# Optimization experiments

Measured on AMD Instinct MI355X. Metric: run time of the kernel, lower is better.

Reference implementation:

```python
import jax, jax.numpy as jnp
import numpy as np

R = 12          # resolution (H = W = G); L = R**3 = 1728
HEADS = 12


def setup_inputs() -> dict:
    key = jax.random.key(0)
    k1, k2, k3 = jax.random.split(key, 3)
    B, L, C = 4, R ** 3, 768
    qkv = jax.random.normal(k1, (3, B, L, C), dtype=jnp.float32)
    lepe_w = jax.random.normal(k2, (C, 1, 3, 3, 3), dtype=jnp.float32) * 0.05
    lepe_b = jax.random.normal(k3, (C,), dtype=jnp.float32) * 0.01
    return {"qkv": qkv, "lepe_w": lepe_w, "lepe_b": lepe_b}


def reference(qkv, lepe_w, lepe_b):
    # qkv: [3, B, L, C]; idx=0 => window == full volume, so attention is dense over L.
    q, k, v = qkv[0], qkv[1], qkv[2]
    B, L, C = q.shape
    hd = C // HEADS
    scale = hd ** -0.5

    # im2cswin with full-volume window preserves token order: [B, L, C] -> [B, H, L, d]
    qh = q.reshape(B, L, HEADS, hd).transpose(0, 2, 1, 3)
    kh = k.reshape(B, L, HEADS, hd).transpose(0, 2, 1, 3)

    # get_lepe: v -> [B, C, R, R, R], depthwise 3x3x3 conv (groups=C)
    v_img = v.transpose(0, 2, 1).reshape(B, C, R, R, R)
    lepe = jax.lax.conv_general_dilated(
        v_img, lepe_w, window_strides=(1, 1, 1), padding="SAME",
        dimension_numbers=("NCDHW", "OIDHW", "NCDHW"), feature_group_count=C,
    ) + lepe_b[None, :, None, None, None]
    lepe = lepe.reshape(B, HEADS, hd, L).transpose(0, 1, 3, 2)   # [B, H, L, d]
    vh = v_img.reshape(B, HEADS, hd, L).transpose(0, 1, 3, 2)    # [B, H, L, d]

    attn = jax.nn.softmax(jnp.einsum("bhqd,bhkd->bhqk", qh * scale, kh), axis=-1)
    out = jnp.einsum("bhqk,bhkd->bhqd", attn, vh) + lepe          # [B, H, L, d]

    # windows2img with full window is an inverse reshape back to [B, L, C]
    return out.transpose(0, 2, 1, 3).reshape(B, L, C)
```

## Files before the change

### kernel.cpp

```cpp
#include <hip/hip_runtime.h>

#define RR 12
#define LL 1728
#define CC 768
#define HEADS 12
#define HD 64
#define BATCH 4

typedef __attribute__((ext_vector_type(8))) short bf8;
typedef __attribute__((ext_vector_type(4))) float f4;

__device__ inline unsigned short f2bf(float x) {
  unsigned int u = __float_as_uint(x);
  return (unsigned short)((u + 0x7FFFu + ((u >> 16) & 1u)) >> 16);
}
__device__ inline unsigned short f2bfr(float x) {
  return (unsigned short)((__float_as_uint(x) + 0x8000u) >> 16);
}

__device__ inline float fast_exp2(float x) {
#if __has_builtin(__builtin_amdgcn_exp2f)
  return __builtin_amdgcn_exp2f(x);
#else
  return exp2f(x);
#endif
}

__device__ inline void gld16(const unsigned short* g, unsigned short* l) {
  __builtin_amdgcn_global_load_lds((const __attribute__((address_space(1))) unsigned int*)g,
                                   (__attribute__((address_space(3))) unsigned int*)l, 16, 0, 0);
}

#define QSCALE 0.1803368801111244f

#define NLEPE 5184
#define NPREP 1296

__global__ __launch_bounds__(256) void combined_kernel(const float* __restrict__ qkv,
                                                       const float* __restrict__ w,
                                                       const float* __restrict__ bias,
                                                       unsigned short* __restrict__ qb,
                                                       unsigned short* __restrict__ kb,
                                                       unsigned short* __restrict__ vT,
                                                       float* __restrict__ out) {
  __shared__ __align__(16) unsigned char smem[27648];
  const int bid = blockIdx.x;
  const int t = threadIdx.x;

  if (bid < NLEPE) {
    const int xg = (bid % 3) * 4;
    const int line = (bid / 3) % 144;
    const int ct = (bid / 432) % 3;
    const int b = bid / 1296;
    const int z = line / RR;
    const int y = line % RR;
    const int c0 = ct * 256;
    const int c = c0 + t;
    float* w_lds = (float*)smem;

    {
      const float* wsrc = w + (size_t)c0 * 27;
#pragma unroll
      for (int i = 0; i < 7; ++i) {
        const int idx = i * 256 + t;
        if (idx < 1728) *(float4*)&w_lds[idx * 4] = *(const float4*)&wsrc[idx * 4];
      }
    }
    __syncthreads();
    float wreg[27];
#pragma unroll
    for (int j = 0; j < 27; ++j) wreg[j] = w_lds[t * 27 + j];

    const float* vb = qkv + ((size_t)(2 * BATCH + b)) * LL * CC + c;
    const float bv = bias[c];
    float acc[4] = {bv, bv, bv, bv};

#pragma unroll
    for (int dz = -1; dz <= 1; ++dz) {
#pragma unroll
      for (int dy = -1; dy <= 1; ++dy) {
        const int zz = z + dz, yy = y + dy;
        const bool lineok = ((unsigned)zz < RR) & ((unsigned)yy < RR);
        const int base = (zz * RR + yy) * RR;
        float v6[6];
#pragma unroll
        for (int p = 0; p < 6; ++p) {
          const int xx = xg - 1 + p;
          const bool ok = lineok & ((unsigned)xx < RR);
          const int lp = ok ? base + xx : 0;
          const float vv = vb[(size_t)lp * CC];
          v6[p] = ok ? vv : 0.f;
        }
        const int jb = ((dz + 1) * 3 + (dy + 1)) * 3;
        const float wL = wreg[jb], wC = wreg[jb + 1], wR = wreg[jb + 2];
#pragma unroll
        for (int i = 0; i < 4; ++i)
          acc[i] += wL * v6[i] + wC * v6[i + 1] + wR * v6[i + 2];
      }
    }
    const size_t obase = ((size_t)b * LL + line * RR + xg) * CC + c;
#pragma unroll
    for (int i = 0; i < 4; ++i) out[obase + (size_t)i * CC] = acc[i];

  } else {
    const int p = bid - NLEPE;
    const int lt = p % 27;
    const int h = (p / 27) % HEADS;
    const int b = p / (27 * HEADS);
    unsigned short* tl = (unsigned short*)smem;

    {
      const int r0 = t >> 4;
      const int c4 = (t & 15) * 4;
#pragma unroll
      for (int pi = 0; pi < 4; ++pi) {
        const int row = lt * 64 + pi * 16 + r0;
        const size_t off = ((size_t)b * LL + row) * CC + h * HD + c4;
        const float4 qv = *(const float4*)(qkv + off);
        ushort4 oq;
        oq.x = f2bf(qv.x * QSCALE); oq.y = f2bf(qv.y * QSCALE);
        oq.z = f2bf(qv.z * QSCALE); oq.w = f2bf(qv.w * QSCALE);
        *(ushort4*)(qb + off) = oq;
        const float4 kv = *(const float4*)(qkv + (size_t)BATCH * LL * CC + off);
        ushort4 ok;
        ok.x = f2bf(kv.x); ok.y = f2bf(kv.y); ok.z = f2bf(kv.z); ok.w = f2bf(kv.w);
        *(ushort4*)(kb + off) = ok;
      }
    }

    const float* vsrc = qkv + ((size_t)(2 * BATCH + b)) * LL * CC;
#pragma unroll
    for (int it = 0; it < 4; ++it) {
      const int idx = it * 256 + t;
      const int lrow = idx >> 4;
      const int c4 = (idx & 15) * 4;
      const float4 vv = *(const float4*)(vsrc + (size_t)(lt * 64 + lrow) * CC + h * HD + c4);
      tl[(c4 + 0) * 65 + lrow] = f2bf(vv.x);
      tl[(c4 + 1) * 65 + lrow] = f2bf(vv.y);
      tl[(c4 + 2) * 65 + lrow] = f2bf(vv.z);
      tl[(c4 + 3) * 65 + lrow] = f2bf(vv.w);
    }
    __syncthreads();
#pragma unroll
    for (int it = 0; it < 4; ++it) {
      const int idx = it * 256 + t;
      const int drow = idx >> 4;
      const int u = idx & 15;
      const int s4 = u * 4;
      const int kbase = (((u >> 3) * 2 + (u & 1)) << 4) + (((u >> 1) & 3) << 2);
      ushort4 o;
      o.x = tl[drow * 65 + kbase + 0];
      o.y = tl[drow * 65 + kbase + 1];
      o.z = tl[drow * 65 + kbase + 2];
      o.w = tl[drow * 65 + kbase + 3];
      *(ushort4*)(vT + (((size_t)(b * HEADS + h) * HD + drow) * LL) + lt * 64 + s4) = o;
    }
  }
}

__global__ __launch_bounds__(256) void attn_kernel(const unsigned short* __restrict__ qb,
                                                   const unsigned short* __restrict__ kb,
                                                   const unsigned short* __restrict__ vT,
                                                   float* __restrict__ out) {
  __shared__ unsigned short k_lds[2][64 * 64];
  __shared__ unsigned short v_lds[2][64 * 64];

  const int qt = blockIdx.x;
  const int h = blockIdx.y;
  const int b = blockIdx.z;
  const int t = threadIdx.x;
  const int lane = t & 63;
  const int wave = t >> 6;
  const int m = lane & 15;
  const int quad = lane >> 4;

  bf8 qf[2];
  {
    const size_t qbase = ((size_t)(b * LL + qt * 64 + wave * 16 + m)) * CC + h * HD;
    qf[0] = *(const bf8*)(qb + qbase + quad * 8);
    qf[1] = *(const bf8*)(qb + qbase + 32 + quad * 8);
  }

  int koff[2], voff[2], ldsb[2];
#pragma unroll
  for (int j = 0; j < 2; ++j) {
    const int cidx = (j * 4 + wave) * 64 + lane;
    const int row = cidx >> 3;
    const int sc = (cidx & 7) ^ (row & 7);
    koff[j] = row * CC + sc * 8;
    voff[j] = row * LL + sc * 8;
    ldsb[j] = (j * 4 + wave) * 512;
  }

  const unsigned short* kgb = kb + (size_t)b * LL * CC + h * HD;
  const unsigned short* vgb = vT + ((size_t)(b * HEADS + h) * HD) * LL;

  gld16(kgb + koff[0], &k_lds[0][ldsb[0]]);
  gld16(kgb + koff[1], &k_lds[0][ldsb[1]]);
  gld16(vgb + voff[0], &v_lds[0][ldsb[0]]);
  gld16(vgb + voff[1], &v_lds[0][ldsb[1]]);

  f4 o_acc[4] = {};
  float psum = 0.f;

#define ATTN_BODY(KT, CUR)                                                              \
  {                                                                                     \
    __syncthreads();            \
    if ((KT) < 26) {                                                                    \
      const size_t ko = (size_t)((KT) + 1) * 64 * CC;                                   \
      const int vo = ((KT) + 1) * 64;                                                   \
      gld16(kgb + ko + koff[0], &k_lds[(CUR) ^ 1][ldsb[0]]);                            \
      gld16(kgb + ko + koff[1], &k_lds[(CUR) ^ 1][ldsb[1]]);                            \
      gld16(vgb + vo + voff[0], &v_lds[(CUR) ^ 1][ldsb[0]]);                            \
      gld16(vgb + vo + voff[1], &v_lds[(CUR) ^ 1][ldsb[1]]);                            \
    }                                                                                   \
    f4 s_acc[4] = {};                                                                   \
    _Pragma("unroll")                                                                   \
    for (int nt = 0; nt < 4; ++nt) {                                                    \
      _Pragma("unroll")                                                                 \
      for (int ks = 0; ks < 2; ++ks) {                                                  \
        const int cc = ((ks * 4 + quad) ^ (m & 7)) * 8;                                 \
        const bf8 kf = *(const bf8*)&k_lds[CUR][(nt * 16 + m) * 64 + cc];               \
        s_acc[nt] = __builtin_amdgcn_mfma_f32_16x16x32_bf16(kf, qf[ks], s_acc[nt], 0, 0, 0); \
      }                                                                                 \
    }                                                                                   \
    bf8 pf[2];                                                                          \
    _Pragma("unroll")                                                                   \
    for (int ks = 0; ks < 2; ++ks) {                                                    \
      union { bf8 v; unsigned int w[4]; } pu;                                           \
      _Pragma("unroll")                                                                 \
      for (int bb = 0; bb < 2; ++bb) {                                                  \
        const int nt = ks * 2 + bb;                                                     \
        const float p0 = fast_exp2(s_acc[nt][0]);                                       \
        const float p1 = fast_exp2(s_acc[nt][1]);                                       \
        const float p2 = fast_exp2(s_acc[nt][2]);                                       \
        const float p3 = fast_exp2(s_acc[nt][3]);                                       \
        psum += (p0 + p1) + (p2 + p3);                                                  \
        pu.w[bb * 2 + 0] = (unsigned int)f2bfr(p0) | ((unsigned int)f2bfr(p1) << 16);   \
        pu.w[bb * 2 + 1] = (unsigned int)f2bfr(p2) | ((unsigned int)f2bfr(p3) << 16);   \
      }                                                                                 \
      pf[ks] = pu.v;                                                                    \
    }                                                                                   \
    _Pragma("unroll")                                                                   \
    for (int nt = 0; nt < 4; ++nt) {                                                    \
      _Pragma("unroll")                                                                 \
      for (int ks = 0; ks < 2; ++ks) {                                                  \
        const int cc = ((ks * 4 + quad) ^ (m & 7)) * 8;                                 \
        const bf8 vf = *(const bf8*)&v_lds[CUR][(nt * 16 + m) * 64 + cc];               \
        o_acc[nt] = __builtin_amdgcn_mfma_f32_16x16x32_bf16(vf, pf[ks], o_acc[nt], 0, 0, 0); \
      }                                                                                 \
    }                                                                                   \
  }

  for (int ktp = 0; ktp < 13; ++ktp) {
    const int kt0 = ktp * 2;
    ATTN_BODY(kt0, 0)
    ATTN_BODY(kt0 + 1, 1)
  }
  ATTN_BODY(26, 0)
#undef ATTN_BODY

  float s = psum;
  s += __shfl_xor(s, 16);
  s += __shfl_xor(s, 32);
  const float inv = 1.0f / s;
  const int rowq = qt * 64 + wave * 16 + m;
  float* op = out + ((size_t)b * LL + rowq) * CC + h * HD + quad * 4;
#pragma unroll
  for (int nt = 0; nt < 4; ++nt) {
    float4 o4 = *(float4*)&op[nt * 16];
    o4.x += o_acc[nt][0] * inv;
    o4.y += o_acc[nt][1] * inv;
    o4.z += o_acc[nt][2] * inv;
    o4.w += o_acc[nt][3] * inv;
    *(float4*)&op[nt * 16] = o4;
  }
}

extern "C" void kernel_launch(void* const* d_in, const int* in_sizes, int n_in,
                              void* d_out, int out_size, void* d_ws, size_t ws_size,
                              hipStream_t stream) {
  (void)in_sizes; (void)n_in; (void)ws_size; (void)out_size;
  const float* qkv = (const float*)d_in[0];
  const float* lepe_w = (const float*)d_in[1];
  const float* lepe_b = (const float*)d_in[2];
  float* out = (float*)d_out;

  const size_t NE = (size_t)BATCH * LL * CC;
  unsigned short* qb = (unsigned short*)d_ws;
  unsigned short* kb = qb + NE;
  unsigned short* vT = kb + NE;

  combined_kernel<<<dim3(NLEPE + NPREP), 256, 0, stream>>>(qkv, lepe_w, lepe_b, qb, kb, vT, out);
  attn_kernel<<<dim3(27, HEADS, BATCH), 256, 0, stream>>>(qb, kb, vT, out);
}
```

Baseline: 193.1 us.

## Process two query sub-tiles per block to reuse K/V tiles

Each block now handles 128 query rows instead of 64, with every wave computing two 16-row sub-tiles against the same K/V tiles loaded into LDS. This halves global K/V traffic and LDS fragment reads per MFMA and gives more independent MFMAs to interleave. In exchange, register use doubles for accumulators, the grid shrinks to fewer blocks (less parallelism and a partially padded last tile with clamped rows), and out-of-range rows are masked on store.

```diff
diff --git a/kernel.cpp b/kernel.cpp
--- a/kernel.cpp
+++ b/kernel.cpp
@@ -174,11 +174,14 @@
   const int m = lane & 15;
   const int quad = lane >> 4;
 
-  bf8 qf[2];
-  {
-    const size_t qbase = ((size_t)(b * LL + qt * 64 + wave * 16 + m)) * CC + h * HD;
-    qf[0] = *(const bf8*)(qb + qbase + quad * 8);
-    qf[1] = *(const bf8*)(qb + qbase + 32 + quad * 8);
+  bf8 qf[2][2];
+#pragma unroll
+  for (int sub = 0; sub < 2; ++sub) {
+    int row = qt * 128 + sub * 64 + wave * 16 + m;
+    row = row < LL ? row : LL - 1;
+    const size_t qbase = ((size_t)(b * LL + row)) * CC + h * HD;
+    qf[sub][0] = *(const bf8*)(qb + qbase + quad * 8);
+    qf[sub][1] = *(const bf8*)(qb + qbase + 32 + quad * 8);
   }
 
   int koff[2], voff[2], ldsb[2];
@@ -200,8 +203,8 @@
   gld16(vgb + voff[0], &v_lds[0][ldsb[0]]);
   gld16(vgb + voff[1], &v_lds[0][ldsb[1]]);
 
-  f4 o_acc[4] = {};
-  float psum = 0.f;
+  f4 o_acc[2][4] = {};
+  float psum[2] = {0.f, 0.f};
 
 #define ATTN_BODY(KT, CUR)                                                              \
   {                                                                                     \
@@ -214,32 +217,36 @@
       gld16(vgb + vo + voff[0], &v_lds[(CUR) ^ 1][ldsb[0]]);                            \
       gld16(vgb + vo + voff[1], &v_lds[(CUR) ^ 1][ldsb[1]]);                            \
     }                                                                                   \
-    f4 s_acc[4] = {};                                                                   \
+    f4 s_acc[2][4] = {};                                                                \
     _Pragma("unroll")                                                                   \
     for (int nt = 0; nt < 4; ++nt) {                                                    \
       _Pragma("unroll")                                                                 \
       for (int ks = 0; ks < 2; ++ks) {                                                  \
         const int cc = ((ks * 4 + quad) ^ (m & 7)) * 8;                                 \
         const bf8 kf = *(const bf8*)&k_lds[CUR][(nt * 16 + m) * 64 + cc];               \
-        s_acc[nt] = __builtin_amdgcn_mfma_f32_16x16x32_bf16(kf, qf[ks], s_acc[nt], 0, 0, 0); \
+        s_acc[0][nt] = __builtin_amdgcn_mfma_f32_16x16x32_bf16(kf, qf[0][ks], s_acc[0][nt], 0, 0, 0); \
+        s_acc[1][nt] = __builtin_amdgcn_mfma_f32_16x16x32_bf16(kf, qf[1][ks], s_acc[1][nt], 0, 0, 0); \
       }                                                                                 \
     }                                                                                   \
-    bf8 pf[2];                                                                          \
+    bf8 pf[2][2];                                                                       \
     _Pragma("unroll")                                                                   \
-    for (int ks = 0; ks < 2; ++ks) {                                                    \
-      union { bf8 v; unsigned int w[4]; } pu;                                           \
+    for (int sub = 0; sub < 2; ++sub) {                                                 \
       _Pragma("unroll")                                                                 \
-      for (int bb = 0; bb < 2; ++bb) {                                                  \
-        const int nt = ks * 2 + bb;                                                     \
-        const float p0 = fast_exp2(s_acc[nt][0]);                                       \
-        const float p1 = fast_exp2(s_acc[nt][1]);                                       \
-        const float p2 = fast_exp2(s_acc[nt][2]);                                       \
-        const float p3 = fast_exp2(s_acc[nt][3]);                                       \
-        psum += (p0 + p1) + (p2 + p3);                                                  \
-        pu.w[bb * 2 + 0] = (unsigned int)f2bfr(p0) | ((unsigned int)f2bfr(p1) << 16);   \
-        pu.w[bb * 2 + 1] = (unsigned int)f2bfr(p2) | ((unsigned int)f2bfr(p3) << 16);   \
+      for (int ks = 0; ks < 2; ++ks) {                                                  \
+        union { bf8 v; unsigned int w[4]; } pu;                                         \
+        _Pragma("unroll")                                                               \
+        for (int bb = 0; bb < 2; ++bb) {                                                \
+          const int nt = ks * 2 + bb;                                                   \
+          const float p0 = fast_exp2(s_acc[sub][nt][0]);                                \
+          const float p1 = fast_exp2(s_acc[sub][nt][1]);                                \
+          const float p2 = fast_exp2(s_acc[sub][nt][2]);                                \
+          const float p3 = fast_exp2(s_acc[sub][nt][3]);                                \
+          psum[sub] += (p0 + p1) + (p2 + p3);                                           \
+          pu.w[bb * 2 + 0] = (unsigned int)f2bfr(p0) | ((unsigned int)f2bfr(p1) << 16); \
+          pu.w[bb * 2 + 1] = (unsigned int)f2bfr(p2) | ((unsigned int)f2bfr(p3) << 16); \
+        }                                                                               \
+        pf[sub][ks] = pu.v;                                                             \
       }                                                                                 \
-      pf[ks] = pu.v;                                                                    \
     }                                                                                   \
     _Pragma("unroll")                                                                   \
     for (int nt = 0; nt < 4; ++nt) {                                                    \
@@ -247,7 +254,8 @@
       for (int ks = 0; ks < 2; ++ks) {                                                  \
         const int cc = ((ks * 4 + quad) ^ (m & 7)) * 8;                                 \
         const bf8 vf = *(const bf8*)&v_lds[CUR][(nt * 16 + m) * 64 + cc];               \
-        o_acc[nt] = __builtin_amdgcn_mfma_f32_16x16x32_bf16(vf, pf[ks], o_acc[nt], 0, 0, 0); \
+        o_acc[0][nt] = __builtin_amdgcn_mfma_f32_16x16x32_bf16(vf, pf[0][ks], o_acc[0][nt], 0, 0, 0); \
+        o_acc[1][nt] = __builtin_amdgcn_mfma_f32_16x16x32_bf16(vf, pf[1][ks], o_acc[1][nt], 0, 0, 0); \
       }                                                                                 \
     }                                                                                   \
   }
@@ -260,20 +268,25 @@
   ATTN_BODY(26, 0)
 #undef ATTN_BODY
 
-  float s = psum;
-  s += __shfl_xor(s, 16);
-  s += __shfl_xor(s, 32);
-  const float inv = 1.0f / s;
-  const int rowq = qt * 64 + wave * 16 + m;
-  float* op = out + ((size_t)b * LL + rowq) * CC + h * HD + quad * 4;
-#pragma unroll
-  for (int nt = 0; nt < 4; ++nt) {
-    float4 o4 = *(float4*)&op[nt * 16];
-    o4.x += o_acc[nt][0] * inv;
-    o4.y += o_acc[nt][1] * inv;
-    o4.z += o_acc[nt][2] * inv;
-    o4.w += o_acc[nt][3] * inv;
-    *(float4*)&op[nt * 16] = o4;
+#pragma unroll
+  for (int sub = 0; sub < 2; ++sub) {
+    float s = psum[sub];
+    s += __shfl_xor(s, 16);
+    s += __shfl_xor(s, 32);
+    const float inv = 1.0f / s;
+    const int rowq = qt * 128 + sub * 64 + wave * 16 + m;
+    if (rowq < LL) {
+      float* op = out + ((size_t)b * LL + rowq) * CC + h * HD + quad * 4;
+#pragma unroll
+      for (int nt = 0; nt < 4; ++nt) {
+        float4 o4 = *(float4*)&op[nt * 16];
+        o4.x += o_acc[sub][nt][0] * inv;
+        o4.y += o_acc[sub][nt][1] * inv;
+        o4.z += o_acc[sub][nt][2] * inv;
+        o4.w += o_acc[sub][nt][3] * inv;
+        *(float4*)&op[nt * 16] = o4;
+      }
+    }
   }
 }
 
@@ -292,5 +305,5 @@
   unsigned short* vT = kb + NE;
 
   combined_kernel<<<dim3(NLEPE + NPREP), 256, 0, stream>>>(qkv, lepe_w, lepe_b, qb, kb, vT, out);
-  attn_kernel<<<dim3(27, HEADS, BATCH), 256, 0, stream>>>(qb, kb, vT, out);
-}
+  attn_kernel<<<dim3(14, HEADS, BATCH), 256, 0, stream>>>(qb, kb, vT, out);
+}
```

New measurement: 191.4 us. Within noise of the previous version (-0.9%).
